# Kernel tuning notes

Hardware: AMD Instinct MI355X
Metric: run time of the kernel (lower is better)

## Reference

```python
import jax, jax.numpy as jnp
import numpy as np

EPS = 1e-5

def conv2d(x, w, b=None, pad=0):
    # x: NCHW, w: OIHW
    y = jax.lax.conv_general_dilated(x, w, (1, 1), [(pad, pad), (pad, pad)],
                                     dimension_numbers=('NCHW', 'OIHW', 'NCHW'))
    if b is not None:
        y = y + b[None, :, None, None]
    return y

def bn(x, g, beta, mean, var):
    scale = g / jnp.sqrt(var + EPS)
    return x * scale[None, :, None, None] + (beta - mean * scale)[None, :, None, None]

def conv_block(x, w, b, g, beta, mean, var):
    # two (conv3x3 + BN + ReLU) stages, params stacked on leading dim 2
    for i in range(2):
        x = jax.nn.relu(bn(conv2d(x, w[i], b[i], pad=1), g[i], beta[i], mean[i], var[i]))
    return x


def setup_inputs() -> dict:
    key = jax.random.key(0)
    ks = jax.random.split(key, 24)
    C, B, H, W = 128, 4, 56, 56
    f32 = jnp.float32
    d = {}
    d['x1'] = jax.random.normal(ks[0], (B, C, H, W), f32)
    d['x2'] = jax.random.normal(ks[1], (B, 4 * C, H, W), f32)
    d['ws'] = jax.random.normal(ks[2], (C, 4 * C, 3, 3), f32) * 0.05
    d['bs'] = jax.random.normal(ks[3], (C,), f32) * 0.05
    d['sg'] = jax.random.uniform(ks[4], (C,), f32)
    d['sbeta'] = jax.random.normal(ks[5], (C,), f32) * 0.05
    d['smean'] = jax.random.normal(ks[6], (C,), f32) * 0.05
    d['svar'] = jax.random.uniform(ks[7], (C,), f32)
    d['wq1'] = jax.random.normal(ks[8], (C, C, 1, 1), f32) * 0.05
    d['wq2'] = jax.random.normal(ks[9], (C, C, 1, 1), f32) * 0.05
    d['v1w'] = jax.random.normal(ks[10], (2, C, C, 3, 3), f32) * 0.05
    d['v1b'] = jax.random.normal(ks[11], (2, C), f32) * 0.05
    d['v1g'] = jax.random.uniform(ks[12], (2, C), f32)
    d['v1beta'] = jax.random.normal(ks[13], (2, C), f32) * 0.05
    d['v1mean'] = jax.random.normal(ks[14], (2, C), f32) * 0.05
    d['v1var'] = jax.random.uniform(ks[15], (2, C), f32)
    d['v2w'] = jax.random.normal(ks[16], (2, C, C, 3, 3), f32) * 0.05
    d['v2b'] = jax.random.normal(ks[17], (2, C), f32) * 0.05
    d['v2g'] = jax.random.uniform(ks[18], (2, C), f32)
    d['v2beta'] = jax.random.normal(ks[19], (2, C), f32) * 0.05
    d['v2mean'] = jax.random.normal(ks[20], (2, C), f32) * 0.05
    d['v2var'] = jax.random.uniform(ks[21], (2, C), f32)
    return d


def reference(x1, x2, ws, bs, sg, sbeta, smean, svar, wq1, wq2,
              v1w, v1b, v1g, v1beta, v1mean, v1var,
              v2w, v2b, v2g, v2beta, v2mean, v2var):
    x2_o = x2
    # conv_s: conv3x3 (4C->C) + BN + ReLU
    x2 = jax.nn.relu(bn(conv2d(x2, ws, bs, pad=1), sg, sbeta, smean, svar))
    B_, C, H, W = x1.shape
    N = H * W
    x1_q = conv2d(x1, wq1)              # [B,C,H,W]
    x2_q = conv2d(x2, wq2)
    x1_v = conv_block(x1, v1w, v1b, v1g, v1beta, v1mean, v1var)
    x2_v = conv_block(x2, v2w, v2b, v2g, v2beta, v2mean, v2var)
    x1_q_flat = x1_q.reshape(B_, C, N)
    x2_q_flat = x2_q.reshape(B_, C, N)
    x2_v_flat = x2_v.reshape(B_, C, N)
    # A[b,n,m] = sum_c x1_q[b,c,n] * x2_q[b,c,m]   -> [B, N1, N2]
    A = jnp.einsum('bcn,bcm->bnm', x1_q_flat, x2_q_flat)
    A = jax.nn.softmax(A, axis=1)                 # softmax over N1 (dim=1)
    # B = softmax(A^T, dim=1) == softmax over N2, then transposed -> [B, N2, N1]
    Bmat = jnp.swapaxes(jax.nn.softmax(A, axis=2), 1, 2)
    # x1_att = bmm(x2_v_flat [B,C,N2], Bmat [B,N2,N1]) -> [B,C,N1]
    x1_att = jnp.einsum('bcm,bmn->bcn', x2_v_flat, Bmat).reshape(B_, C, H, W)
    input1_att = x1_att + x1
    input2_att = x2_o
    return (input1_att, input2_att)
```

## Files before the change

### kernel.cpp

```cpp
#include <hip/hip_runtime.h>
#include <cstdint>
#include <cstddef>

using bfr8 = __attribute__((ext_vector_type(8))) short;
using sh4  = __attribute__((ext_vector_type(4))) short;
using fx4  = __attribute__((ext_vector_type(4))) float;

#define DI __device__ __forceinline__
#define MFMA16(a,b,c) __builtin_amdgcn_mfma_f32_16x16x32_bf16((a),(b),(c),0,0,0)

DI short f2bf(float f){
  unsigned u = __float_as_uint(f);
  return (short)((u + 0x7fffu + ((u >> 16) & 1u)) >> 16);
}
DI float bf2f(short s){
  return __uint_as_float(((unsigned)(unsigned short)s) << 16);
}
DI fx4 fzero(){ fx4 z; z[0]=0.f; z[1]=0.f; z[2]=0.f; z[3]=0.f; return z; }

__global__ void prep_kernel(
    const float* __restrict__ x1, const float* __restrict__ x2,
    const float* __restrict__ wsw, const float* __restrict__ bs,
    const float* __restrict__ sg, const float* __restrict__ sbeta,
    const float* __restrict__ smean, const float* __restrict__ svar,
    const float* __restrict__ wq1, const float* __restrict__ wq2,
    const float* __restrict__ v2w, const float* __restrict__ v2bias,
    const float* __restrict__ v2g, const float* __restrict__ v2beta,
    const float* __restrict__ v2mean, const float* __restrict__ v2var,
    short* __restrict__ x2bf, short* __restrict__ x1T,
    short* __restrict__ wsbf, short* __restrict__ wv2a, short* __restrict__ wv2b,
    short* __restrict__ wq1b, short* __restrict__ wq2b,
    float* __restrict__ consts, float* __restrict__ out1copy)
{
  const int gsz = gridDim.x * blockDim.x;
  const int gid = blockIdx.x * blockDim.x + threadIdx.x;

  for (int i = gid; i < 1605632; i += gsz){
    float4 v = ((const float4*)x2)[i];
    ((float4*)out1copy)[i] = v;
    sh4 o; o[0]=f2bf(v.x); o[1]=f2bf(v.y); o[2]=f2bf(v.z); o[3]=f2bf(v.w);
    ((sh4*)x2bf)[i] = o;
  }
  for (int t = gid; t < 200704; t += gsz){
    int g = t & 15; int nn = t >> 4;
    int b = nn / 3136, n = nn - b*3136;
    bfr8 o;
    #pragma unroll
    for (int k = 0; k < 8; ++k)
      o[k] = f2bf(x1[(size_t)(b*128 + g*8 + k)*3136 + n]);
    *(bfr8*)&x1T[((size_t)(b*3136) + n)*128 + g*8] = o;
  }
  for (int i = gid; i < 589824; i += gsz){
    int ci = i & 511; int tap = (i >> 9) % 9; int co = i / 4608;
    wsbf[i] = f2bf(wsw[(size_t)(co*512 + ci)*9 + tap]);
  }
  for (int i = gid; i < 294912; i += gsz){
    int s = i / 147456; int r = i - s*147456;
    int ci = r & 127; int tap = (r >> 7) % 9; int co = r / 1152;
    float v = v2w[(size_t)((s*128 + co)*128 + ci)*9 + tap];
    (s ? wv2b : wv2a)[r] = f2bf(v);
  }
  for (int i = gid; i < 16384; i += gsz){
    wq1b[i] = f2bf(wq1[i]); wq2b[i] = f2bf(wq2[i]);
  }
  for (int c = gid; c < 128; c += gsz){
    float a = sg[c] * rsqrtf(svar[c] + 1e-5f);
    consts[c]       = a;
    consts[128 + c] = (bs[c] - smean[c]) * a + sbeta[c];
    float a0 = v2g[c] * rsqrtf(v2var[c] + 1e-5f);
    consts[256 + c] = a0;
    consts[384 + c] = (v2bias[c] - v2mean[c]) * a0 + v2beta[c];
    float a1 = v2g[128+c] * rsqrtf(v2var[128+c] + 1e-5f);
    consts[512 + c] = a1;
    consts[640 + c] = (v2bias[128+c] - v2mean[128+c]) * a1 + v2beta[128+c];
  }
}

template<int CIN, int NCIB>
__global__ __launch_bounds__(256, 2) void conv3x3_split_kernel(
    const short* __restrict__ xin, const short* __restrict__ wt,
    float* __restrict__ pout)
{
  __shared__ short xs[4*58*40];
  __shared__ short wsh[9*64*40];

  const int tid = threadIdx.x;
  const int w = tid >> 6, lane = tid & 63, l15 = lane & 15, blk = lane >> 4;
  const int bid = blockIdx.x;
  const int rt = bid % 28, cog = (bid / 28) & 1, b = bid / 56;
  const int r0 = rt * 2;
  const int split = blockIdx.y;
  const int cib0 = split * NCIB;
  float* pbase = pout + (size_t)split * 1605632;

  int pixoff[7];
  #pragma unroll
  for (int pf = 0; pf < 7; ++pf){
    int p = pf*16 + l15;
    int pr = (p >= 56) ? 1 : 0;
    int pc = p - pr*56;
    pixoff[pf] = (pr*58 + pc)*40 + 8*blk;
  }
  const int wlo = (w*16 + l15)*40 + 8*blk;

  fx4 acc[7];
  #pragma unroll
  for (int pf = 0; pf < 7; ++pf) acc[pf] = fzero();

  for (int ci = 0; ci < NCIB; ++ci){
    const int cib = cib0 + ci;
    __syncthreads();
    #pragma unroll
    for (int it = 0; it < 4; ++it){
      int q = it*256 + tid;
      if (q < 928){
        int col = q % 58; int cg8 = (q/58) & 3; int r = q / 232;
        int grow = r0 - 1 + r;
        int gcol = col - 1;
        bfr8 v;
        if (grow >= 0 && grow < 56 && gcol >= 0 && gcol < 56){
          #pragma unroll
          for (int k = 0; k < 8; ++k)
            v[k] = xin[(size_t)(b*CIN + cib*32 + cg8*8 + k)*3136 + grow*56 + gcol];
        } else {
          #pragma unroll
          for (int k = 0; k < 8; ++k) v[k] = 0;
        }
        *(bfr8*)&xs[(r*58 + col)*40 + cg8*8] = v;
      }
    }
    #pragma unroll
    for (int it = 0; it < 9; ++it){
      int q = it*256 + tid;
      int jj = q & 3; int tap = (q >> 2) % 9; int co = q / 36;
      bfr8 wv = *(const bfr8*)&wt[(size_t)((cog*64 + co)*9 + tap)*CIN + cib*32 + jj*8];
      *(bfr8*)&wsh[(tap*64 + co)*40 + jj*8] = wv;
    }
    __syncthreads();
    #pragma unroll
    for (int tap = 0; tap < 9; ++tap){
      bfr8 af = *(const bfr8*)&wsh[tap*64*40 + wlo];
      const int toff = ((tap/3)*58 + (tap%3))*40;
      #pragma unroll
      for (int pf = 0; pf < 7; ++pf){
        bfr8 bf = *(const bfr8*)&xs[pixoff[pf] + toff];
        acc[pf] = MFMA16(af, bf, acc[pf]);
      }
    }
  }
  #pragma unroll
  for (int rr = 0; rr < 4; ++rr){
    int co = cog*64 + w*16 + 4*blk + rr;
    #pragma unroll
    for (int pf = 0; pf < 7; ++pf){
      int n = r0*56 + pf*16 + l15;
      pbase[(size_t)(b*128 + co)*3136 + n] = acc[pf][rr];
    }
  }
}

template<int NS, bool TSTORE>
__global__ __launch_bounds__(256, 4) void conv_combine_kernel(
    const float* __restrict__ p, const float* __restrict__ alpha,
    const float* __restrict__ bconst,
    short* __restrict__ yout, short* __restrict__ youtT)
{
  __shared__ short lt[64][66];
  const int t = threadIdx.x;
  const int bid = blockIdx.x;
  const int nt = bid % 49, cog = (bid / 49) & 1, b = bid / 98;
  const int co0 = cog*64, n0 = nt*64;
  const int coL = t >> 4, ncL = (t & 15) * 4;

  #pragma unroll
  for (int rep = 0; rep < 4; ++rep){
    int co = co0 + rep*16 + coL;
    size_t base = ((size_t)(b*128) + co)*3136 + n0 + ncL;
    float4 s = *(const float4*)&p[base];
    #pragma unroll
    for (int sp = 1; sp < NS; ++sp){
      float4 a = *(const float4*)&p[(size_t)sp*1605632 + base];
      s.x += a.x; s.y += a.y; s.z += a.z; s.w += a.w;
    }
    float al = alpha[co], bc = bconst[co];
    sh4 o;
    o[0] = f2bf(fmaxf(s.x*al + bc, 0.f));
    o[1] = f2bf(fmaxf(s.y*al + bc, 0.f));
    o[2] = f2bf(fmaxf(s.z*al + bc, 0.f));
    o[3] = f2bf(fmaxf(s.w*al + bc, 0.f));
    *(sh4*)&yout[base] = o;
    if (TSTORE) *(sh4*)&lt[rep*16 + coL][ncL] = o;
  }
  if (TSTORE){
    __syncthreads();
    #pragma unroll
    for (int rep = 0; rep < 4; ++rep){
      int nn = rep*16 + (t >> 4);
      int coc = (t & 15) * 4;
      sh4 v;
      #pragma unroll
      for (int j = 0; j < 4; ++j) v[j] = lt[coc + j][nn];
      *(sh4*)&youtT[((size_t)(b*3136) + n0 + nn)*128 + co0 + coc] = v;
    }
  }
}

template<int CIN, bool TSTORE>
__global__ __launch_bounds__(256, 2) void conv3x3_kernel(
    const short* __restrict__ xin, const short* __restrict__ wt,
    const float* __restrict__ alpha, const float* __restrict__ bconst,
    short* __restrict__ yout, short* __restrict__ youtT)
{
  __shared__ short xs[4*58*40];
  __shared__ short wsh[9*64*40];

  const int tid = threadIdx.x;
  const int w = tid >> 6, lane = tid & 63, l15 = lane & 15, blk = lane >> 4;
  const int bid = blockIdx.x;
  const int rt = bid % 28, cog = (bid / 28) & 1, b = bid / 56;
  const int r0 = rt * 2;

  int pixoff[7];
  #pragma unroll
  for (int pf = 0; pf < 7; ++pf){
    int p = pf*16 + l15;
    int pr = (p >= 56) ? 1 : 0;
    int pc = p - pr*56;
    pixoff[pf] = (pr*58 + pc)*40 + 8*blk;
  }
  const int wlo = (w*16 + l15)*40 + 8*blk;

  fx4 acc[7];
  #pragma unroll
  for (int pf = 0; pf < 7; ++pf) acc[pf] = fzero();

  for (int cib = 0; cib < CIN/32; ++cib){
    __syncthreads();
    #pragma unroll
    for (int it = 0; it < 4; ++it){
      int q = it*256 + tid;
      if (q < 928){
        int col = q % 58; int cg8 = (q/58) & 3; int r = q / 232;
        int grow = r0 - 1 + r;
        int gcol = col - 1;
        bfr8 v;
        if (grow >= 0 && grow < 56 && gcol >= 0 && gcol < 56){
          #pragma unroll
          for (int k = 0; k < 8; ++k)
            v[k] = xin[(size_t)(b*CIN + cib*32 + cg8*8 + k)*3136 + grow*56 + gcol];
        } else {
          #pragma unroll
          for (int k = 0; k < 8; ++k) v[k] = 0;
        }
        *(bfr8*)&xs[(r*58 + col)*40 + cg8*8] = v;
      }
    }
    #pragma unroll
    for (int it = 0; it < 9; ++it){
      int q = it*256 + tid;
      int jj = q & 3; int tap = (q >> 2) % 9; int co = q / 36;
      bfr8 wv = *(const bfr8*)&wt[(size_t)((cog*64 + co)*9 + tap)*CIN + cib*32 + jj*8];
      *(bfr8*)&wsh[(tap*64 + co)*40 + jj*8] = wv;
    }
    __syncthreads();
    #pragma unroll
    for (int tap = 0; tap < 9; ++tap){
      bfr8 af = *(const bfr8*)&wsh[tap*64*40 + wlo];
      const int toff = ((tap/3)*58 + (tap%3))*40;
      #pragma unroll
      for (int pf = 0; pf < 7; ++pf){
        bfr8 bf = *(const bfr8*)&xs[pixoff[pf] + toff];
        acc[pf] = MFMA16(af, bf, acc[pf]);
      }
    }
  }
  #pragma unroll
  for (int rr = 0; rr < 4; ++rr){
    int co = cog*64 + w*16 + 4*blk + rr;
    float al = alpha[co], bc = bconst[co];
    #pragma unroll
    for (int pf = 0; pf < 7; ++pf){
      float v = fmaxf(acc[pf][rr]*al + bc, 0.f);
      short sv = f2bf(v);
      int n = r0*56 + pf*16 + l15;
      yout[(size_t)(b*128 + co)*3136 + n] = sv;
// ... 50 lines not shown
      qa[mf][ks] = *(const bfr8*)&q2t[((size_t)(b*3136) + m0 + mf*16 + l15)*128 + ks*32 + 8*blk];

  float vmax[4][4], vsum[4][4];
  #pragma unroll
  for (int mf = 0; mf < 4; ++mf)
    #pragma unroll
    for (int rr = 0; rr < 4; ++rr){ vmax[mf][rr] = -1e30f; vsum[mf][rr] = 0.f; }

  bfr8 qb[4], qbn[4];
  #pragma unroll
  for (int ks = 0; ks < 4; ++ks)
    qb[ks] = *(const bfr8*)&q1t[((size_t)(b*3136) + ns*784 + w*16 + l15)*128 + ks*32 + 8*blk];

  for (int c = w; c < 49; c += 4){
    const int cn = c + 4;
    if (cn < 49){
      #pragma unroll
      for (int ks = 0; ks < 4; ++ks)
        qbn[ks] = *(const bfr8*)&q1t[((size_t)(b*3136) + ns*784 + cn*16 + l15)*128 + ks*32 + 8*blk];
    }
    fx4 acc[4];
    #pragma unroll
    for (int mf = 0; mf < 4; ++mf) acc[mf] = fzero();
    #pragma unroll
    for (int ks = 0; ks < 4; ++ks)
      #pragma unroll
      for (int mf = 0; mf < 4; ++mf)
        acc[mf] = MFMA16(qa[mf][ks], qb[ks], acc[mf]);
    #pragma unroll
    for (int mf = 0; mf < 4; ++mf)
      #pragma unroll
      for (int rr = 0; rr < 4; ++rr){
        float s = acc[mf][rr];
        float nm = fmaxf(vmax[mf][rr], s);
        vsum[mf][rr] = vsum[mf][rr]*__expf(vmax[mf][rr]-nm) + __expf(s-nm);
        vmax[mf][rr] = nm;
      }
    #pragma unroll
    for (int ks = 0; ks < 4; ++ks) qb[ks] = qbn[ks];
  }
  #pragma unroll
  for (int d = 1; d < 16; d <<= 1){
    #pragma unroll
    for (int mf = 0; mf < 4; ++mf)
      #pragma unroll
      for (int rr = 0; rr < 4; ++rr){
        float om = __shfl_xor(vmax[mf][rr], d);
        float os = __shfl_xor(vsum[mf][rr], d);
        float M = fmaxf(vmax[mf][rr], om);
        vsum[mf][rr] = vsum[mf][rr]*__expf(vmax[mf][rr]-M) + os*__expf(om-M);
        vmax[mf][rr] = M;
      }
  }
  if (l15 == 0){
    const size_t base = ((size_t)(b*16 + ns*4 + w))*3136 + m0;
    #pragma unroll
    for (int mf = 0; mf < 4; ++mf)
      #pragma unroll
      for (int rr = 0; rr < 4; ++rr){
        pmax[base + mf*16 + 4*blk + rr] = vmax[mf][rr];
        psum[base + mf*16 + 4*blk + rr] = vsum[mf][rr];
      }
  }
}

__global__ void lse_merge_kernel(
    const float* __restrict__ pmax, const float* __restrict__ psum,
    float* __restrict__ Lm)
{
  int t = blockIdx.x*256 + threadIdx.x;
  if (t >= 12544) return;
  int b = t / 3136, m = t - b*3136;
  float M = -1e30f;
  #pragma unroll
  for (int r = 0; r < 16; ++r)
    M = fmaxf(M, pmax[((size_t)(b*16 + r))*3136 + m]);
  float S = 0.f;
  #pragma unroll
  for (int r = 0; r < 16; ++r){
    size_t i = ((size_t)(b*16 + r))*3136 + m;
    S += psum[i]*__expf(pmax[i] - M);
  }
  Lm[t] = M + __logf(S);
}

__global__ __launch_bounds__(256, 3) void attn3_kernel(
    const short* __restrict__ q1t, const short* __restrict__ q2t,
    const short* __restrict__ x2v, const float* __restrict__ Lm,
    float* __restrict__ part, float* __restrict__ rpart)
{
  __shared__ short q2sh[64*128];
  __shared__ short xsh[128*64];
  __shared__ short plds[4*16*72];
  __shared__ float lmsh[448];
  const int tid = threadIdx.x, w = tid >> 6, lane = tid & 63;
  const int l15 = lane & 15, blk = lane >> 4;
  const int bid = blockIdx.x;
  const int ms = bid % 7, nt = (bid / 7) % 49, b = bid / 343;
  const int m0 = ms*448;
  const int n0w = nt*64 + w*16;

  if (tid < 112)
    ((float4*)lmsh)[tid] = ((const float4*)(Lm + b*3136 + m0))[tid];

  bfr8 qb[4];
  #pragma unroll
  for (int ks = 0; ks < 4; ++ks)
    qb[ks] = *(const bfr8*)&q1t[((size_t)(b*3136) + n0w + l15)*128 + ks*32 + 8*blk];

  bfr8 stq[4], stx[4];
  auto issue = [&](int m0c){
    #pragma unroll
    for (int j = 0; j < 4; ++j){
      int u = tid + 256*j;
      stq[j] = *(const bfr8*)&q2t[((size_t)(b*3136) + m0c + (u>>4))*128 + (u&15)*8];
      stx[j] = *(const bfr8*)&x2v[((size_t)(b*128) + (u>>3))*3136 + m0c + (u&7)*8];
    }
  };
  auto write_stage = [&](){
    #pragma unroll
    for (int j = 0; j < 4; ++j){
      int u = tid + 256*j;
      int qrow = u >> 4;
      *(bfr8*)((char*)q2sh + ((qrow*256 + (u&15)*16) ^ ((qrow&7)<<4))) = stq[j];
      int xrow = u >> 3;
      *(bfr8*)((char*)xsh + ((xrow*128 + (u&7)*16) ^ ((xrow&7)<<4))) = stx[j];
    }
  };

  fx4 pacc[8];
  #pragma unroll
  for (int cf = 0; cf < 8; ++cf) pacc[cf] = fzero();
  float rsum = 0.f;

  issue(m0);

  for (int c = 0; c < 7; ++c){
    __syncthreads();
    write_stage();
    if (c < 6) issue(m0 + (c+1)*64);
    __syncthreads();

    fx4 acc[4];
    #pragma unroll
    for (int mf = 0; mf < 4; ++mf) acc[mf] = fzero();
    #pragma unroll
    for (int ks = 0; ks < 4; ++ks){
      #pragma unroll
      for (int mf = 0; mf < 4; ++mf){
        const int row = mf*16 + l15;
        bfr8 qv = *(const bfr8*)((const char*)q2sh +
                    ((row*256 + ks*64 + 16*blk) ^ ((row&7)<<4)));
        acc[mf] = MFMA16(qv, qb[ks], acc[mf]);
      }
    }

    #pragma unroll
    for (int mf = 0; mf < 4; ++mf){
      fx4 lv = *(const fx4*)&lmsh[c*64 + mf*16 + 4*blk];
      sh4 pk;
      #pragma unroll
      for (int rr = 0; rr < 4; ++rr){
        float a1 = __expf(acc[mf][rr] - lv[rr]);
        float p  = __expf(a1);
        rsum += p;
        pk[rr] = f2bf(p);
      }
      *(sh4*)&plds[(w*16 + l15)*72 + mf*16 + 4*blk] = pk;
    }
    #pragma unroll
    for (int ks2 = 0; ks2 < 2; ++ks2){
      bfr8 pb = *(const bfr8*)&plds[(w*16 + l15)*72 + ks2*32 + 8*blk];
      #pragma unroll
      for (int cf = 0; cf < 8; ++cf){
        const int row = cf*16 + l15;
        bfr8 av = *(const bfr8*)((const char*)xsh +
                    ((row*128 + ks2*64 + 16*blk) ^ ((row&7)<<4)));
        pacc[cf] = MFMA16(av, pb, pacc[cf]);
      }
    }
  }

  rsum += __shfl_xor(rsum, 16);
  rsum += __shfl_xor(rsum, 32);
  if (lane < 16)
    rpart[((size_t)(ms*4 + b))*3136 + n0w + l15] = rsum;

  #pragma unroll
  for (int cf = 0; cf < 8; ++cf)
    #pragma unroll
    for (int rr = 0; rr < 4; ++rr){
      int cc = cf*16 + 4*blk + rr;
      part[(((size_t)(ms*4 + b))*128 + cc)*3136 + n0w + l15] = pacc[cf][rr];
    }
}

__global__ void rtot_kernel(const float* __restrict__ rpart,
                            float* __restrict__ rinv)
{
  int t = blockIdx.x*256 + threadIdx.x;
  if (t >= 12544) return;
  int b = t / 3136, n = t - b*3136;
  float s = 0.f;
  #pragma unroll
  for (int ms = 0; ms < 7; ++ms)
    s += rpart[((size_t)(ms*4 + b))*3136 + n];
  rinv[t] = 1.0f / s;
}

__global__ __launch_bounds__(256, 8) void attn_combine_kernel(
    const float* __restrict__ part, const float* __restrict__ rinv,
    const float* __restrict__ x1, float* __restrict__ out0)
{
  int t = blockIdx.x*256 + threadIdx.x;
  int n4 = t % 784; int rest = t / 784;
  int cc = rest & 127; int b = rest >> 7;
  const float4* p4 = (const float4*)part;
  float4 s = {0.f,0.f,0.f,0.f};
  #pragma unroll
  for (int ms = 0; ms < 7; ++ms){
    float4 v = p4[(((size_t)(ms*4 + b))*128 + cc)*784 + n4];
    s.x += v.x; s.y += v.y; s.z += v.z; s.w += v.w;
  }
  float4 rv = ((const float4*)rinv)[b*784 + n4];
  size_t xi = ((size_t)(b*128) + cc)*784 + n4;
  float4 xv = ((const float4*)x1)[xi];
  float4 o;
  o.x = s.x*rv.x + xv.x; o.y = s.y*rv.y + xv.y;
  o.z = s.z*rv.z + xv.z; o.w = s.w*rv.w + xv.w;
  ((float4*)out0)[xi] = o;
}

__global__ __launch_bounds__(256, 2) void colstats_kernel(
    const short* __restrict__ q1t, const short* __restrict__ q2t,
    float* __restrict__ Lm)
{
  __shared__ float smax[4][16];
  __shared__ float ssum[4][16];
  const int tid = threadIdx.x, w = tid >> 6, lane = tid & 63;
  const int l15 = lane & 15, blk = lane >> 4;
  const int b = blockIdx.x / 196, m0 = (blockIdx.x % 196) * 16;

  bfr8 bfr[4];
  #pragma unroll
  for (int ks = 0; ks < 4; ++ks)
    bfr[ks] = *(const bfr8*)&q2t[((size_t)(b*3136) + m0 + l15)*128 + ks*32 + 8*blk];

  float vmax = -1e30f, vsum = 0.f;

  for (int nc = w; nc < 196; nc += 4){
    fx4 acc = fzero();
    #pragma unroll
    for (int ks = 0; ks < 4; ++ks){
      bfr8 af = *(const bfr8*)&q1t[((size_t)(b*3136) + nc*16 + l15)*128 + ks*32 + 8*blk];
      acc = MFMA16(af, bfr[ks], acc);
// ... 108 lines not shown
      int c = cf*16 + 4*blk + rr;
      size_t idx = (size_t)(b*128 + c)*3136 + n;
      out0[idx] = v*rinv + x1[idx];
    }
  }
}

extern "C" void kernel_launch(void* const* d_in, const int* in_sizes, int n_in,
                              void* d_out, int out_size, void* d_ws, size_t ws_size,
                              hipStream_t stream)
{
  (void)in_sizes; (void)n_in; (void)out_size;
  const float* x1     = (const float*)d_in[0];
  const float* x2     = (const float*)d_in[1];
  const float* wsw    = (const float*)d_in[2];
  const float* bs     = (const float*)d_in[3];
  const float* sg     = (const float*)d_in[4];
  const float* sbeta  = (const float*)d_in[5];
  const float* smean  = (const float*)d_in[6];
  const float* svar   = (const float*)d_in[7];
  const float* wq1    = (const float*)d_in[8];
  const float* wq2    = (const float*)d_in[9];
  const float* v2w    = (const float*)d_in[16];
  const float* v2bias = (const float*)d_in[17];
  const float* v2g    = (const float*)d_in[18];
  const float* v2beta = (const float*)d_in[19];
  const float* v2mean = (const float*)d_in[20];
  const float* v2var  = (const float*)d_in[21];

  char* ws = (char*)d_ws;
  auto al = [](size_t x){ return (x + 255) & ~(size_t)255; };

  const size_t sz_nc    = al((size_t)1605632*2);
  const size_t sz_x2bf  = al((size_t)6422528*2);
  const size_t sz_Lm    = al((size_t)12544*4);
  const size_t sz_lsep  = al((size_t)16*12544*4);
  const size_t sz_rp    = al((size_t)28*12544*4);
  const size_t sz_cst   = al((size_t)768*4);
  const size_t sz_part  = al((size_t)7*1605632*4);
  const size_t sz_wsbf  = al((size_t)589824*2);
  const size_t sz_wv2   = al((size_t)147456*2);
  const size_t sz_wq    = al((size_t)16384*2);

  short *x2bf, *x1T, *wsbf, *wv2a, *wv2b, *wq1b, *wq2b;
  short *x2s, *x2sT, *q1t, *q2t, *v2t, *x2v;
  float *consts, *Lm;
  float *pmax = nullptr, *psum = nullptr, *part = nullptr;
  float *rpart = nullptr, *rinv = nullptr, *pbuf = nullptr;

  size_t off = 0;
  const size_t o_x2v = off;  off += sz_nc;
  const size_t o_q1t = off;  off += sz_nc;
  const size_t o_q2t = off;  off += sz_nc;
  const size_t o_Lm  = off;  off += sz_Lm;
  const size_t o_pmx = off;  off += sz_lsep;
  const size_t o_psm = off;  off += sz_lsep;
  const size_t o_rp  = off;  off += sz_rp;
  const size_t o_ri  = off;  off += sz_Lm;
  const size_t o_cst = off;  off += sz_cst;
  const size_t o_prt = off;  off += sz_part;
  const size_t o_x2b = off;  off += sz_x2bf;
  const size_t o_x1T = off;  off += sz_nc;
  const size_t o_xsT = off;  off += sz_nc;
  const size_t o_x2s = off;  off += sz_nc;
  const size_t o_v2t = off;  off += sz_nc;
  const size_t o_wsb = off;  off += sz_wsbf;
  const size_t o_wva = off;  off += sz_wv2;
  const size_t o_wvb = off;  off += sz_wv2;
  const size_t o_wq1 = off;  off += sz_wq;
  const size_t o_wq2 = off;  off += sz_wq;
  const size_t fast_need = off;
  const bool fast = (ws_size >= fast_need);

  if (fast){
    x2v    = (short*)(ws + o_x2v);
    q1t    = (short*)(ws + o_q1t);
    q2t    = (short*)(ws + o_q2t);
    Lm     = (float*)(ws + o_Lm);
    pmax   = (float*)(ws + o_pmx);
    psum   = (float*)(ws + o_psm);
    rpart  = (float*)(ws + o_rp);
    rinv   = (float*)(ws + o_ri);
    consts = (float*)(ws + o_cst);
    part   = (float*)(ws + o_prt);
    pbuf   = (float*)(ws + o_prt);
    x2bf   = (short*)(ws + o_x2b);
    x1T    = (short*)(ws + o_x1T);
    x2sT   = (short*)(ws + o_xsT);
    x2s    = (short*)(ws + o_x2s);
    v2t    = (short*)(ws + o_v2t);
    wsbf   = (short*)(ws + o_wsb);
    wv2a   = (short*)(ws + o_wva);
    wv2b   = (short*)(ws + o_wvb);
    wq1b   = (short*)(ws + o_wq1);
    wq2b   = (short*)(ws + o_wq2);
  } else {
    size_t o = 0;
    auto bump = [&](size_t bytes)->char*{ char* p = ws + o; o += al(bytes); return p; };
    x2bf   = (short*)bump((size_t)6422528*2);
    x1T    = (short*)bump((size_t)1605632*2);
    wsbf   = (short*)bump((size_t)589824*2);
    wv2a   = (short*)bump((size_t)147456*2);
    wv2b   = (short*)bump((size_t)147456*2);
    wq1b   = (short*)bump((size_t)16384*2);
    wq2b   = (short*)bump((size_t)16384*2);
    consts = (float*)bump((size_t)768*4);
    x2s    = (short*)bump((size_t)1605632*2);
    x2sT   = (short*)bump((size_t)1605632*2);
    q1t    = (short*)bump((size_t)1605632*2);
    q2t    = (short*)bump((size_t)1605632*2);
    v2t    = (short*)bump((size_t)1605632*2);
    x2v    = (short*)bump((size_t)1605632*2);
    Lm     = (float*)bump((size_t)12544*4);
  }

  float* out0 = (float*)d_out;
  float* out1 = out0 + 1605632;

  prep_kernel<<<2048, 256, 0, stream>>>(x1, x2, wsw, bs, sg, sbeta, smean, svar,
      wq1, wq2, v2w, v2bias, v2g, v2beta, v2mean, v2var,
      x2bf, x1T, wsbf, wv2a, wv2b, wq1b, wq2b, consts, out1);

  if (fast){
    conv3x3_split_kernel<512, 4><<<dim3(224,4), 256, 0, stream>>>(x2bf, wsbf, pbuf);
    conv_combine_kernel<4, true ><<<392, 256, 0, stream>>>(pbuf, consts,       consts + 128, x2s, x2sT);
    qproj_kernel<<<784, 256, 0, stream>>>(x1T,  wq1b, q1t);
    qproj_kernel<<<784, 256, 0, stream>>>(x2sT, wq2b, q2t);
    conv3x3_split_kernel<128, 2><<<dim3(224,2), 256, 0, stream>>>(x2s, wv2a, pbuf);
    conv_combine_kernel<2, false><<<392, 256, 0, stream>>>(pbuf, consts + 256, consts + 384, v2t, nullptr);
    conv3x3_split_kernel<128, 2><<<dim3(224,2), 256, 0, stream>>>(v2t, wv2b, pbuf);
    conv_combine_kernel<2, false><<<392, 256, 0, stream>>>(pbuf, consts + 512, consts + 640, x2v, nullptr);
    lse_kernel<<<784, 256, 0, stream>>>(q1t, q2t, pmax, psum);
    lse_merge_kernel<<<49, 256, 0, stream>>>(pmax, psum, Lm);
    attn3_kernel<<<1372, 256, 0, stream>>>(q1t, q2t, x2v, Lm, part, rpart);
    rtot_kernel<<<49, 256, 0, stream>>>(rpart, rinv);
    attn_combine_kernel<<<1568, 256, 0, stream>>>(part, rinv, x1, out0);
  } else {
    conv3x3_kernel<512, true ><<<224, 256, 0, stream>>>(x2bf, wsbf, consts, consts + 128, x2s, x2sT);
    qproj_kernel<<<784, 256, 0, stream>>>(x1T,  wq1b, q1t);
    qproj_kernel<<<784, 256, 0, stream>>>(x2sT, wq2b, q2t);
    conv3x3_kernel<128, false><<<224, 256, 0, stream>>>(x2s, wv2a, consts + 256, consts + 384, v2t, nullptr);
    conv3x3_kernel<128, false><<<224, 256, 0, stream>>>(v2t, wv2b, consts + 512, consts + 640, x2v, nullptr);
    colstats_kernel<<<784, 256, 0, stream>>>(q1t, q2t, Lm);
    attn_kernel<<<784, 256, 0, stream>>>(q1t, q2t, x2v, Lm, x1, out0);
  }
}
```

Baseline: 216.1 us.

## Use channel-last bf16 activations for convs and bf16 attention partials

```diff
diff --git a/kernel.cpp b/kernel.cpp
--- a/kernel.cpp
+++ b/kernel.cpp
@@ -17,6 +17,8 @@
   return __uint_as_float(((unsigned)(unsigned short)s) << 16);
 }
 DI fx4 fzero(){ fx4 z; z[0]=0.f; z[1]=0.f; z[2]=0.f; z[3]=0.f; return z; }
+DI bfr8 bzero(){ bfr8 z; 
+  z[0]=0; z[1]=0; z[2]=0; z[3]=0; z[4]=0; z[5]=0; z[6]=0; z[7]=0; return z; }
 
 __global__ void prep_kernel(
     const float* __restrict__ x1, const float* __restrict__ x2,
@@ -30,7 +32,7 @@
     short* __restrict__ x2bf, short* __restrict__ x1T,
     short* __restrict__ wsbf, short* __restrict__ wv2a, short* __restrict__ wv2b,
     short* __restrict__ wq1b, short* __restrict__ wq2b,
-    float* __restrict__ consts, float* __restrict__ out1copy)
+    float* __restrict__ consts, float* __restrict__ out1copy, int legacy)
 {
   const int gsz = gridDim.x * blockDim.x;
   const int gid = blockIdx.x * blockDim.x + threadIdx.x;
@@ -38,17 +40,21 @@
   for (int i = gid; i < 1605632; i += gsz){
     float4 v = ((const float4*)x2)[i];
     ((float4*)out1copy)[i] = v;
-    sh4 o; o[0]=f2bf(v.x); o[1]=f2bf(v.y); o[2]=f2bf(v.z); o[3]=f2bf(v.w);
-    ((sh4*)x2bf)[i] = o;
-  }
-  for (int t = gid; t < 200704; t += gsz){
-    int g = t & 15; int nn = t >> 4;
-    int b = nn / 3136, n = nn - b*3136;
-    bfr8 o;
-    #pragma unroll
-    for (int k = 0; k < 8; ++k)
-      o[k] = f2bf(x1[(size_t)(b*128 + g*8 + k)*3136 + n]);
-    *(bfr8*)&x1T[((size_t)(b*3136) + n)*128 + g*8] = o;
+    if (legacy){
+      sh4 o; o[0]=f2bf(v.x); o[1]=f2bf(v.y); o[2]=f2bf(v.z); o[3]=f2bf(v.w);
+      ((sh4*)x2bf)[i] = o;
+    }
+  }
+  if (legacy){
+    for (int t = gid; t < 200704; t += gsz){
+      int g = t & 15; int nn = t >> 4;
+      int b = nn / 3136, n = nn - b*3136;
+      bfr8 o;
+      #pragma unroll
+      for (int k = 0; k < 8; ++k)
+        o[k] = f2bf(x1[(size_t)(b*128 + g*8 + k)*3136 + n]);
+      *(bfr8*)&x1T[((size_t)(b*3136) + n)*128 + g*8] = o;
+    }
   }
   for (int i = gid; i < 589824; i += gsz){
     int ci = i & 511; int tap = (i >> 9) % 9; int co = i / 4608;
@@ -76,9 +82,37 @@
   }
 }
 
+template<int C>
+__global__ __launch_bounds__(256, 4) void transpose_cn_kernel(
+    const float* __restrict__ in, short* __restrict__ out)
+{
+  __shared__ float t[32][65];
+  const int tid = threadIdx.x, bid = blockIdx.x;
+  const int nt = bid % 49, cg = (bid / 49) % (C/32), b = bid / (49*(C/32));
+  const int n0 = nt*64, c0 = cg*32;
+
+  #pragma unroll
+  for (int j = 0; j < 2; ++j){
+    int u = tid + 256*j;
+    int row = u >> 4, col4 = u & 15;
+    float4 v = *(const float4*)&in[((size_t)(b*C) + c0 + row)*3136 + n0 + col4*4];
+    t[row][col4*4+0] = v.x; t[row][col4*4+1] = v.y;
+    t[row][col4*4+2] = v.z; t[row][col4*4+3] = v.w;
+  }
+  __syncthreads();
+  {
+    int n = tid >> 2, cg8 = tid & 3;
+    bfr8 o;
+    #pragma unroll
+    for (int k = 0; k < 8; ++k) o[k] = f2bf(t[cg8*8 + k][n]);
+    *(bfr8*)&out[((size_t)(b*3136) + n0 + n)*C + c0 + cg8*8] = o;
+  }
+}
+
 template<int CIN, int NCIB>
 __global__ __launch_bounds__(256, 2) void conv3x3_split_kernel(
-    const short* __restrict__ xin, const short* __restrict__ wt,
+    const short* __restrict__ xin,
+    const short* __restrict__ wt,
     float* __restrict__ pout)
 {
   __shared__ short xs[4*58*40];
@@ -89,9 +123,8 @@
   const int bid = blockIdx.x;
   const int rt = bid % 28, cog = (bid / 28) & 1, b = bid / 56;
   const int r0 = rt * 2;
-  const int split = blockIdx.y;
-  const int cib0 = split * NCIB;
-  float* pbase = pout + (size_t)split * 1605632;
+  const int cib0 = blockIdx.y * NCIB;
+  float* pbase = pout + (size_t)blockIdx.y * 1605632;
 
   int pixoff[7];
   #pragma unroll
@@ -103,12 +136,145 @@
   }
   const int wlo = (w*16 + l15)*40 + 8*blk;
 
+  int in_act[4], in_val[4], in_lds[4], in_go[4];
+  #pragma unroll
+  for (int it = 0; it < 4; ++it){
+    int q = it*256 + tid;
+    int cg8 = q & 3, col = (q >> 2) % 58, r = q / 232;
+    int grow = r0 - 1 + r, gcol = col - 1;
+    in_act[it] = (q < 928);
+    in_val[it] = in_act[it] && grow >= 0 && grow < 56 && gcol >= 0 && gcol < 56;
+    in_lds[it] = (r*58 + col)*40 + cg8*8;
+    int gr = in_val[it] ? grow : 0, gc = in_val[it] ? gcol : 0;
+    in_go[it] = (b*3136 + gr*56 + gc)*CIN + cib0*32 + cg8*8;
+  }
+  int wt_lds[9], wt_go[9];
+  #pragma unroll
+  for (int it = 0; it < 9; ++it){
+    int q = it*256 + tid;
+    int jj = q & 3, tap = (q >> 2) % 9, co = q / 36;
+    wt_lds[it] = (tap*64 + co)*40 + jj*8;
+    wt_go[it] = ((cog*64 + co)*9 + tap)*CIN + cib0*32 + jj*8;
+  }
+
   fx4 acc[7];
   #pragma unroll
   for (int pf = 0; pf < 7; ++pf) acc[pf] = fzero();
 
   for (int ci = 0; ci < NCIB; ++ci){
-    const int cib = cib0 + ci;
+    __syncthreads();
+    #pragma unroll
+    for (int it = 0; it < 4; ++it){
+      if (in_act[it]){
+        bfr8 v = bzero();
+        if (in_val[it]) v = *(const bfr8*)&xin[in_go[it]];
+        *(bfr8*)&xs[in_lds[it]] = v;
+        in_go[it] += 32;
+      }
+    }
+    #pragma unroll
+    for (int it = 0; it < 9; ++it){
+      *(bfr8*)&wsh[wt_lds[it]] = *(const bfr8*)&wt[wt_go[it]];
+      wt_go[it] += 32;
+    }
+    __syncthreads();
+    #pragma unroll
+    for (int tap = 0; tap < 9; ++tap){
+      bfr8 af = *(const bfr8*)&wsh[tap*64*40 + wlo];
+      const int toff = ((tap/3)*58 + (tap%3))*40;
+      #pragma unroll
+      for (int pf = 0; pf < 7; ++pf){
+        bfr8 bf = *(const bfr8*)&xs[pixoff[pf] + toff];
+        acc[pf] = MFMA16(af, bf, acc[pf]);
+      }
+    }
+  }
+  #pragma unroll
+  for (int rr = 0; rr < 4; ++rr){
+    int co = cog*64 + w*16 + 4*blk + rr;
+    #pragma unroll
+    for (int pf = 0; pf < 7; ++pf){
+      int n = r0*56 + pf*16 + l15;
+      pbase[(size_t)(b*128 + co)*3136 + n] = acc[pf][rr];
+    }
+  }
+}
+
+template<int NS, int MODE>
+__global__ __launch_bounds__(256, 4) void conv_combine_kernel(
+    const float* __restrict__ p, const float* __restrict__ alpha,
+    const float* __restrict__ bconst, short* __restrict__ yout)
+{
+  __shared__ short lt[64][66];
+  const int t = threadIdx.x;
+  const int bid = blockIdx.x;
+  const int nt = bid % 49, cog = (bid / 49) & 1, b = bid / 98;
+  const int co0 = cog*64, n0 = nt*64;
+  const int coL = t >> 4, ncL = (t & 15) * 4;
+
+  #pragma unroll
+  for (int rep = 0; rep < 4; ++rep){
+    int co = co0 + rep*16 + coL;
+    size_t base = ((size_t)(b*128) + co)*3136 + n0 + ncL;
+    float4 s = *(const float4*)&p[base];
+    #pragma unroll
+    for (int sp = 1; sp < NS; ++sp){
+      float4 a = *(const float4*)&p[(size_t)sp*1605632 + base];
+      s.x += a.x; s.y += a.y; s.z += a.z; s.w += a.w;
+    }
+    float al = alpha[co], bc = bconst[co];
+    sh4 o;
+    o[0] = f2bf(fmaxf(s.x*al + bc, 0.f));
+    o[1] = f2bf(fmaxf(s.y*al + bc, 0.f));
+    o[2] = f2bf(fmaxf(s.z*al + bc, 0.f));
+    o[3] = f2bf(fmaxf(s.w*al + bc, 0.f));
+    if (MODE == 0) *(sh4*)&yout[base] = o;
+    else           *(sh4*)&lt[rep*16 + coL][ncL] = o;
+  }
+  if (MODE == 1){
+    __syncthreads();
+    #pragma unroll
+    for (int rep = 0; rep < 4; ++rep){
+      int nn = rep*16 + (t >> 4);
+      int coc = (t & 15) * 4;
+      sh4 v;
+      #pragma unroll
+      for (int j = 0; j < 4; ++j) v[j] = lt[coc + j][nn];
+      *(sh4*)&yout[((size_t)(b*3136) + n0 + nn)*128 + co0 + coc] = v;
+    }
+  }
+}
+
+template<int CIN, bool TSTORE>
+__global__ __launch_bounds__(256, 2) void conv3x3_kernel(
+    const short* __restrict__ xin, const short* __restrict__ wt,
+    const float* __restrict__ alpha, const float* __restrict__ bconst,
+    short* __restrict__ yout, short* __restrict__ youtT)
+{
+  __shared__ short xs[4*58*40];
+  __shared__ short wsh[9*64*40];
+
+  const int tid = threadIdx.x;
+  const int w = tid >> 6, lane = tid & 63, l15 = lane & 15, blk = lane >> 4;
+  const int bid = blockIdx.x;
+  const int rt = bid % 28, cog = (bid / 28) & 1, b = bid / 56;
+  const int r0 = rt * 2;
+
+  int pixoff[7];
+  #pragma unroll
+  for (int pf = 0; pf < 7; ++pf){
+    int p = pf*16 + l15;
+    int pr = (p >= 56) ? 1 : 0;
+    int pc = p - pr*56;
+    pixoff[pf] = (pr*58 + pc)*40 + 8*blk;
+  }
+  const int wlo = (w*16 + l15)*40 + 8*blk;
+
+  fx4 acc[7];
+  #pragma unroll
+  for (int pf = 0; pf < 7; ++pf) acc[pf] = fzero();
+
+  for (int cib = 0; cib < CIN/32; ++cib){
     __syncthreads();
     #pragma unroll
     for (int it = 0; it < 4; ++it){
@@ -117,140 +283,11 @@
         int col = q % 58; int cg8 = (q/58) & 3; int r = q / 232;
         int grow = r0 - 1 + r;
         int gcol = col - 1;
-        bfr8 v;
+        bfr8 v = bzero();
         if (grow >= 0 && grow < 56 && gcol >= 0 && gcol < 56){
           #pragma unroll
           for (int k = 0; k < 8; ++k)
             v[k] = xin[(size_t)(b*CIN + cib*32 + cg8*8 + k)*3136 + grow*56 + gcol];
-        } else {
-          #pragma unroll
-          for (int k = 0; k < 8; ++k) v[k] = 0;
-        }
-        *(bfr8*)&xs[(r*58 + col)*40 + cg8*8] = v;
-      }
-    }
-    #pragma unroll
-    for (int it = 0; it < 9; ++it){
-      int q = it*256 + tid;
-      int jj = q & 3; int tap = (q >> 2) % 9; int co = q / 36;
-      bfr8 wv = *(const bfr8*)&wt[(size_t)((cog*64 + co)*9 + tap)*CIN + cib*32 + jj*8];
-      *(bfr8*)&wsh[(tap*64 + co)*40 + jj*8] = wv;
-    }
-    __syncthreads();
-    #pragma unroll
-    for (int tap = 0; tap < 9; ++tap){
-      bfr8 af = *(const bfr8*)&wsh[tap*64*40 + wlo];
-      const int toff = ((tap/3)*58 + (tap%3))*40;
-      #pragma unroll
-      for (int pf = 0; pf < 7; ++pf){
-        bfr8 bf = *(const bfr8*)&xs[pixoff[pf] + toff];
-        acc[pf] = MFMA16(af, bf, acc[pf]);
-      }
-    }
-  }
-  #pragma unroll
-  for (int rr = 0; rr < 4; ++rr){
-    int co = cog*64 + w*16 + 4*blk + rr;
-    #pragma unroll
-    for (int pf = 0; pf < 7; ++pf){
-      int n = r0*56 + pf*16 + l15;
-      pbase[(size_t)(b*128 + co)*3136 + n] = acc[pf][rr];
-    }
-  }
-}
-
-template<int NS, bool TSTORE>
-__global__ __launch_bounds__(256, 4) void conv_combine_kernel(
-    const float* __restrict__ p, const float* __restrict__ alpha,
-    const float* __restrict__ bconst,
-    short* __restrict__ yout, short* __restrict__ youtT)
-{
-  __shared__ short lt[64][66];
-  const int t = threadIdx.x;
-  const int bid = blockIdx.x;
-  const int nt = bid % 49, cog = (bid / 49) & 1, b = bid / 98;
-  const int co0 = cog*64, n0 = nt*64;
-  const int coL = t >> 4, ncL = (t & 15) * 4;
-
-  #pragma unroll
-  for (int rep = 0; rep < 4; ++rep){
-    int co = co0 + rep*16 + coL;
-    size_t base = ((size_t)(b*128) + co)*3136 + n0 + ncL;
-    float4 s = *(const float4*)&p[base];
-    #pragma unroll
-    for (int sp = 1; sp < NS; ++sp){
-      float4 a = *(const float4*)&p[(size_t)sp*1605632 + base];
-      s.x += a.x; s.y += a.y; s.z += a.z; s.w += a.w;
-    }
-    float al = alpha[co], bc = bconst[co];
-    sh4 o;
-    o[0] = f2bf(fmaxf(s.x*al + bc, 0.f));
-    o[1] = f2bf(fmaxf(s.y*al + bc, 0.f));
-    o[2] = f2bf(fmaxf(s.z*al + bc, 0.f));
-    o[3] = f2bf(fmaxf(s.w*al + bc, 0.f));
-    *(sh4*)&yout[base] = o;
-    if (TSTORE) *(sh4*)&lt[rep*16 + coL][ncL] = o;
-  }
-  if (TSTORE){
-    __syncthreads();
-    #pragma unroll
-    for (int rep = 0; rep < 4; ++rep){
-      int nn = rep*16 + (t >> 4);
-      int coc = (t & 15) * 4;
-      sh4 v;
-      #pragma unroll
-      for (int j = 0; j < 4; ++j) v[j] = lt[coc + j][nn];
-      *(sh4*)&youtT[((size_t)(b*3136) + n0 + nn)*128 + co0 + coc] = v;
-    }
-  }
-}
-
-template<int CIN, bool TSTORE>
-__global__ __launch_bounds__(256, 2) void conv3x3_kernel(
-    const short* __restrict__ xin, const short* __restrict__ wt,
-    const float* __restrict__ alpha, const float* __restrict__ bconst,
-    short* __restrict__ yout, short* __restrict__ youtT)
-{
-  __shared__ short xs[4*58*40];
-  __shared__ short wsh[9*64*40];
-
-  const int tid = threadIdx.x;
-  const int w = tid >> 6, lane = tid & 63, l15 = lane & 15, blk = lane >> 4;
-  const int bid = blockIdx.x;
-  const int rt = bid % 28, cog = (bid / 28) & 1, b = bid / 56;
-  const int r0 = rt * 2;
-
-  int pixoff[7];
-  #pragma unroll
-  for (int pf = 0; pf < 7; ++pf){
-    int p = pf*16 + l15;
-    int pr = (p >= 56) ? 1 : 0;
-    int pc = p - pr*56;
-    pixoff[pf] = (pr*58 + pc)*40 + 8*blk;
-  }
-  const int wlo = (w*16 + l15)*40 + 8*blk;
-
-  fx4 acc[7];
-  #pragma unroll
-  for (int pf = 0; pf < 7; ++pf) acc[pf] = fzero();
-
-  for (int cib = 0; cib < CIN/32; ++cib){
-    __syncthreads();
-    #pragma unroll
-    for (int it = 0; it < 4; ++it){
-      int q = it*256 + tid;
-      if (q < 928){
-        int col = q % 58; int cg8 = (q/58) & 3; int r = q / 232;
-        int grow = r0 - 1 + r;
-        int gcol = col - 1;
-        bfr8 v;
-        if (grow >= 0 && grow < 56 && gcol >= 0 && gcol < 56){
-          #pragma unroll
-          for (int k = 0; k < 8; ++k)
-            v[k] = xin[(size_t)(b*CIN + cib*32 + cg8*8 + k)*3136 + grow*56 + gcol];
-        } else {
-          #pragma unroll
-          for (int k = 0; k < 8; ++k) v[k] = 0;
         }
         *(bfr8*)&xs[(r*58 + col)*40 + cg8*8] = v;
       }
@@ -367,9 +404,13 @@
       #pragma unroll
       for (int rr = 0; rr < 4; ++rr){
         float s = acc[mf][rr];
-        float nm = fmaxf(vmax[mf][rr], s);
-        vsum[mf][rr] = vsum[mf][rr]*__expf(vmax[mf][rr]-nm) + __expf(s-nm);
-        vmax[mf][rr] = nm;
+        float d = s - vmax[mf][rr];
+        float e = __expf(-fabsf(d));
+        bool up = d > 0.f;
+        float mlt = up ? e : 1.f;
+        float add = up ? 1.f : e;
+        vsum[mf][rr] = vsum[mf][rr]*mlt + add;
+        vmax[mf][rr] = fmaxf(vmax[mf][rr], s);
       }
     #pragma unroll
     for (int ks = 0; ks < 4; ++ks) qb[ks] = qbn[ks];
@@ -419,14 +460,14 @@
   Lm[t] = M + __logf(S);
 }
 
-__global__ __launch_bounds__(256, 3) void attn3_kernel(
+__global__ __launch_bounds__(256, 4) void attn3_kernel(
     const short* __restrict__ q1t, const short* __restrict__ q2t,
     const short* __restrict__ x2v, const float* __restrict__ Lm,
-    float* __restrict__ part, float* __restrict__ rpart)
-{
-  __shared__ short q2sh[64*128];
-  __shared__ short xsh[128*64];
-  __shared__ short plds[4*16*72];
+    short* __restrict__ part, float* __restrict__ rpart)
+{
+  __shared__ short q2sh[32*128];
+  __shared__ short xsh[128*32];
+  __shared__ short plds[4*16*40];
   __shared__ float lmsh[448];
   const int tid = threadIdx.x, w = tid >> 6, lane = tid & 63;
   const int l15 = lane & 15, blk = lane >> 4;
@@ -443,23 +484,23 @@
   for (int ks = 0; ks < 4; ++ks)
     qb[ks] = *(const bfr8*)&q1t[((size_t)(b*3136) + n0w + l15)*128 + ks*32 + 8*blk];
 
-  bfr8 stq[4], stx[4];
+  bfr8 stq[2], stx[2];
   auto issue = [&](int m0c){
     #pragma unroll
-    for (int j = 0; j < 4; ++j){
+    for (int j = 0; j < 2; ++j){
       int u = tid + 256*j;
       stq[j] = *(const bfr8*)&q2t[((size_t)(b*3136) + m0c + (u>>4))*128 + (u&15)*8];
-      stx[j] = *(const bfr8*)&x2v[((size_t)(b*128) + (u>>3))*3136 + m0c + (u&7)*8];
+      stx[j] = *(const bfr8*)&x2v[((size_t)(b*128) + (u>>2))*3136 + m0c + (u&3)*8];
     }
   };
   auto write_stage = [&](){
     #pragma unroll
-    for (int j = 0; j < 4; ++j){
+    for (int j = 0; j < 2; ++j){
       int u = tid + 256*j;
       int qrow = u >> 4;
       *(bfr8*)((char*)q2sh + ((qrow*256 + (u&15)*16) ^ ((qrow&7)<<4))) = stq[j];
-      int xrow = u >> 3;
-      *(bfr8*)((char*)xsh + ((xrow*128 + (u&7)*16) ^ ((xrow&7)<<4))) = stx[j];
+      int xrow = u >> 2;
+      *(bfr8*)((char*)xsh + ((xrow*64 + (u&3)*16) ^ ((xrow&7)<<4))) = stx[j];
     }
   };
 
@@ -470,19 +511,18 @@
 
   issue(m0);
 
-  for (int c = 0; c < 7; ++c){
+  for (int c = 0; c < 14; ++c){
     __syncthreads();
     write_stage();
-    if (c < 6) issue(m0 + (c+1)*64);
+    if (c < 13) issue(m0 + (c+1)*32);
     __syncthreads();
 
-    fx4 acc[4];
-    #pragma unroll
-    for (int mf = 0; mf < 4; ++mf) acc[mf] = fzero();
+    fx4 acc[2];
+    acc[0] = fzero(); acc[1] = fzero();
     #pragma unroll
     for (int ks = 0; ks < 4; ++ks){
       #pragma unroll
-      for (int mf = 0; mf < 4; ++mf){
+      for (int mf = 0; mf < 2; ++mf){
         const int row = mf*16 + l15;
         bfr8 qv = *(const bfr8*)((const char*)q2sh +
                     ((row*256 + ks*64 + 16*blk) ^ ((row&7)<<4)));
@@ -491,8 +531,8 @@
     }
 
     #pragma unroll
-    for (int mf = 0; mf < 4; ++mf){
-      fx4 lv = *(const fx4*)&lmsh[c*64 + mf*16 + 4*blk];
+    for (int mf = 0; mf < 2; ++mf){
+      fx4 lv = *(const fx4*)&lmsh[c*32 + mf*16 + 4*blk];
       sh4 pk;
       #pragma unroll
       for (int rr = 0; rr < 4; ++rr){
@@ -501,18 +541,15 @@
         rsum += p;
         pk[rr] = f2bf(p);
       }
-      *(sh4*)&plds[(w*16 + l15)*72 + mf*16 + 4*blk] = pk;
-    }
-    #pragma unroll
-    for (int ks2 = 0; ks2 < 2; ++ks2){
-      bfr8 pb = *(const bfr8*)&plds[(w*16 + l15)*72 + ks2*32 + 8*blk];
-      #pragma unroll
-      for (int cf = 0; cf < 8; ++cf){
-        const int row = cf*16 + l15;
-        bfr8 av = *(const bfr8*)((const char*)xsh +
-                    ((row*128 + ks2*64 + 16*blk) ^ ((row&7)<<4)));
-        pacc[cf] = MFMA16(av, pb, pacc[cf]);
-      }
+      *(sh4*)&plds[(w*16 + l15)*40 + mf*16 + 4*blk] = pk;
+    }
+    bfr8 pb = *(const bfr8*)&plds[(w*16 + l15)*40 + 8*blk];
+    #pragma unroll
+    for (int cf = 0; cf < 8; ++cf){
+      const int row = cf*16 + l15;
+      bfr8 av = *(const bfr8*)((const char*)xsh +
+                  ((row*64 + 16*blk) ^ ((row&7)<<4)));
+      pacc[cf] = MFMA16(av, pb, pacc[cf]);
     }
   }
 
@@ -526,7 +563,7 @@
     #pragma unroll
     for (int rr = 0; rr < 4; ++rr){
       int cc = cf*16 + 4*blk + rr;
-      part[(((size_t)(ms*4 + b))*128 + cc)*3136 + n0w + l15] = pacc[cf][rr];
+      part[(((size_t)(ms*4 + b))*128 + cc)*3136 + n0w + l15] = f2bf(pacc[cf][rr]);
     }
 }
 
@@ -544,18 +581,17 @@
 }
 
 __global__ __launch_bounds__(256, 8) void attn_combine_kernel(
-    const float* __restrict__ part, const float* __restrict__ rinv,
+    const short* __restrict__ part, const float* __restrict__ rinv,
     const float* __restrict__ x1, float* __restrict__ out0)
 {
   int t = blockIdx.x*256 + threadIdx.x;
   int n4 = t % 784; int rest = t / 784;
   int cc = rest & 127; int b = rest >> 7;
-  const float4* p4 = (const float4*)part;
   float4 s = {0.f,0.f,0.f,0.f};
   #pragma unroll
   for (int ms = 0; ms < 7; ++ms){
-    float4 v = p4[(((size_t)(ms*4 + b))*128 + cc)*784 + n4];
-    s.x += v.x; s.y += v.y; s.z += v.z; s.w += v.w;
+    sh4 v = *(const sh4*)&part[((((size_t)(ms*4 + b))*128 + cc)*3136) + n4*4];
+    s.x += bf2f(v[0]); s.y += bf2f(v[1]); s.z += bf2f(v[2]); s.w += bf2f(v[3]);
   }
   float4 rv = ((const float4*)rinv)[b*784 + n4];
   size_t xi = ((size_t)(b*128) + cc)*784 + n4;
@@ -730,110 +766,107 @@
   auto al = [](size_t x){ return (x + 255) & ~(size_t)255; };
 
   const size_t sz_nc    = al((size_t)1605632*2);
-  const size_t sz_x2bf  = al((size_t)6422528*2);
+  const size_t sz_x2T   = al((size_t)6422528*2);
   const size_t sz_Lm    = al((size_t)12544*4);
   const size_t sz_lsep  = al((size_t)16*12544*4);
   const size_t sz_rp    = al((size_t)28*12544*4);
   const size_t sz_cst   = al((size_t)768*4);
-  const size_t sz_part  = al((size_t)7*1605632*4);
+  const size_t sz_part  = al((size_t)7*1605632*2);
+  const size_t sz_pbuf  = al((size_t)4*1605632*4);
   const size_t sz_wsbf  = al((size_t)589824*2);
   const size_t sz_wv2   = al((size_t)147456*2);
   const size_t sz_wq    = al((size_t)16384*2);
-
-  short *x2bf, *x1T, *wsbf, *wv2a, *wv2b, *wq1b, *wq2b;
-  short *x2s, *x2sT, *q1t, *q2t, *v2t, *x2v;
-  float *consts, *Lm;
-  float *pmax = nullptr, *psum = nullptr, *part = nullptr;
-  float *rpart = nullptr, *rinv = nullptr, *pbuf = nullptr;
 
   size_t off = 0;
   const size_t o_x2v = off;  off += sz_nc;
   const size_t o_q1t = off;  off += sz_nc;
   const size_t o_q2t = off;  off += sz_nc;
+  const size_t o_x1T = off;  off += sz_nc;
+  const size_t o_x2s = off;  off += sz_nc;
+  const size_t o_v2t = off;  off += sz_nc;
   const size_t o_Lm  = off;  off += sz_Lm;
   const size_t o_pmx = off;  off += sz_lsep;
   const size_t o_psm = off;  off += sz_lsep;
   const size_t o_rp  = off;  off += sz_rp;
   const size_t o_ri  = off;  off += sz_Lm;
   const size_t o_cst = off;  off += sz_cst;
-  const size_t o_prt = off;  off += sz_part;
-  const size_t o_x2b = off;  off += sz_x2bf;
-  const size_t o_x1T = off;  off += sz_nc;
-  const size_t o_xsT = off;  off += sz_nc;
-  const size_t o_x2s = off;  off += sz_nc;
-  const size_t o_v2t = off;  off += sz_nc;
   const size_t o_wsb = off;  off += sz_wsbf;
   const size_t o_wva = off;  off += sz_wv2;
   const size_t o_wvb = off;  off += sz_wv2;
   const size_t o_wq1 = off;  off += sz_wq;
   const size_t o_wq2 = off;  off += sz_wq;
+  const size_t o_x2T = off;  off += sz_x2T;
+  const size_t o_prt = off;  off += (sz_part > sz_pbuf ? sz_part : sz_pbuf);
   const size_t fast_need = off;
   const bool fast = (ws_size >= fast_need);
 
-  if (fast){
-    x2v    = (short*)(ws + o_x2v);
-    q1t    = (short*)(ws + o_q1t);
-    q2t    = (short*)(ws + o_q2t);
-    Lm     = (float*)(ws + o_Lm);
-    pmax   = (float*)(ws + o_pmx);
-    psum   = (float*)(ws + o_psm);
-    rpart  = (float*)(ws + o_rp);
-    rinv   = (float*)(ws + o_ri);
-    consts = (float*)(ws + o_cst);
-    part   = (float*)(ws + o_prt);
-    pbuf   = (float*)(ws + o_prt);
-    x2bf   = (short*)(ws + o_x2b);
-    x1T    = (short*)(ws + o_x1T);
-    x2sT   = (short*)(ws + o_xsT);
-    x2s    = (short*)(ws + o_x2s);
-    v2t    = (short*)(ws + o_v2t);
-    wsbf   = (short*)(ws + o_wsb);
-    wv2a   = (short*)(ws + o_wva);
-    wv2b   = (short*)(ws + o_wvb);
-    wq1b   = (short*)(ws + o_wq1);
-    wq2b   = (short*)(ws + o_wq2);
-  } else {
-    size_t o = 0;
-    auto bump = [&](size_t bytes)->char*{ char* p = ws + o; o += al(bytes); return p; };
-    x2bf   = (short*)bump((size_t)6422528*2);
-    x1T    = (short*)bump((size_t)1605632*2);
-    wsbf   = (short*)bump((size_t)589824*2);
-    wv2a   = (short*)bump((size_t)147456*2);
-    wv2b   = (short*)bump((size_t)147456*2);
-    wq1b   = (short*)bump((size_t)16384*2);
-    wq2b   = (short*)bump((size_t)16384*2);
-    consts = (float*)bump((size_t)768*4);
-    x2s    = (short*)bump((size_t)1605632*2);
-    x2sT   = (short*)bump((size_t)1605632*2);
-    q1t    = (short*)bump((size_t)1605632*2);
-    q2t    = (short*)bump((size_t)1605632*2);
-    v2t    = (short*)bump((size_t)1605632*2);
-    x2v    = (short*)bump((size_t)1605632*2);
-    Lm     = (float*)bump((size_t)12544*4);
-  }
-
   float* out0 = (float*)d_out;
   float* out1 = out0 + 1605632;
 
-  prep_kernel<<<2048, 256, 0, stream>>>(x1, x2, wsw, bs, sg, sbeta, smean, svar,
-      wq1, wq2, v2w, v2bias, v2g, v2beta, v2mean, v2var,
-      x2bf, x1T, wsbf, wv2a, wv2b, wq1b, wq2b, consts, out1);
-
   if (fast){
-    conv3x3_split_kernel<512, 4><<<dim3(224,4), 256, 0, stream>>>(x2bf, wsbf, pbuf);
-    conv_combine_kernel<4, true ><<<392, 256, 0, stream>>>(pbuf, consts,       consts + 128, x2s, x2sT);
-    qproj_kernel<<<784, 256, 0, stream>>>(x1T,  wq1b, q1t);
-    qproj_kernel<<<784, 256, 0, stream>>>(x2sT, wq2b, q2t);
+    short* x2v  = (short*)(ws + o_x2v);
+    short* q1t  = (short*)(ws + o_q1t);
+    short* q2t  = (short*)(ws + o_q2t);
+    short* x1T  = (short*)(ws + o_x1T);
+    short* x2s  = (short*)(ws + o_x2s);
+    short* v2t  = (short*)(ws + o_v2t);
+    float* Lm   = (float*)(ws + o_Lm);
+    float* pmax = (float*)(ws + o_pmx);
+    float* psum = (float*)(ws + o_psm);
+    float* rpart= (float*)(ws + o_rp);
+    float* rinv = (float*)(ws + o_ri);
+    float* consts = (float*)(ws + o_cst);
+    short* wsbf = (short*)(ws + o_wsb);
+    short* wv2a = (short*)(ws + o_wva);
+    short* wv2b = (short*)(ws + o_wvb);
+    short* wq1b = (short*)(ws + o_wq1);
+    short* wq2b = (short*)(ws + o_wq2);
+    short* x2T  = (short*)(ws + o_x2T);
+    short* part = (short*)(ws + o_prt);
+    float* pbuf = (float*)(ws + o_prt);
+
+    prep_kernel<<<2048, 256, 0, stream>>>(x1, x2, wsw, bs, sg, sbeta, smean, svar,
+        wq1, wq2, v2w, v2bias, v2g, v2beta, v2mean, v2var,
+        nullptr, nullptr, wsbf, wv2a, wv2b, wq1b, wq2b, consts, out1, 0);
+    transpose_cn_kernel<512><<<3136, 256, 0, stream>>>(x2, x2T);
+    transpose_cn_kernel<128><<<784, 256, 0, stream>>>(x1, x1T);
+
+    conv3x3_split_kernel<512, 4><<<dim3(224,4), 256, 0, stream>>>(x2T, wsbf, pbuf);
+    conv_combine_kernel<4, 1><<<392, 256, 0, stream>>>(pbuf, consts,       consts + 128, x2s);
+    qproj_kernel<<<784, 256, 0, stream>>>(x1T, wq1b, q1t);
+    qproj_kernel<<<784, 256, 0, stream>>>(x2s, wq2b, q2t);
     conv3x3_split_kernel<128, 2><<<dim3(224,2), 256, 0, stream>>>(x2s, wv2a, pbuf);
-    conv_combine_kernel<2, false><<<392, 256, 0, stream>>>(pbuf, consts + 256, consts + 384, v2t, nullptr);
+    conv_combine_kernel<2, 1><<<392, 256, 0, stream>>>(pbuf, consts + 256, consts + 384, v2t);
     conv3x3_split_kernel<128, 2><<<dim3(224,2), 256, 0, stream>>>(v2t, wv2b, pbuf);
-    conv_combine_kernel<2, false><<<392, 256, 0, stream>>>(pbuf, consts + 512, consts + 640, x2v, nullptr);
+    conv_combine_kernel<2, 0><<<392, 256, 0, stream>>>(pbuf, consts + 512, consts + 640, x2v);
+
     lse_kernel<<<784, 256, 0, stream>>>(q1t, q2t, pmax, psum);
     lse_merge_kernel<<<49, 256, 0, stream>>>(pmax, psum, Lm);
     attn3_kernel<<<1372, 256, 0, stream>>>(q1t, q2t, x2v, Lm, part, rpart);
     rtot_kernel<<<49, 256, 0, stream>>>(rpart, rinv);
     attn_combine_kernel<<<1568, 256, 0, stream>>>(part, rinv, x1, out0);
   } else {
+    size_t o = 0;
+    auto bump = [&](size_t bytes)->char*{ char* p = ws + o; o += al(bytes); return p; };
+    short* x2bf   = (short*)bump((size_t)6422528*2);
+    short* x1T    = (short*)bump((size_t)1605632*2);
+    short* wsbf   = (short*)bump((size_t)589824*2);
+    short* wv2a   = (short*)bump((size_t)147456*2);
+    short* wv2b   = (short*)bump((size_t)147456*2);
+    short* wq1b   = (short*)bump((size_t)16384*2);
+    short* wq2b   = (short*)bump((size_t)16384*2);
+    float* consts = (float*)bump((size_t)768*4);
+    short* x2s    = (short*)bump((size_t)1605632*2);
+    short* x2sT   = (short*)bump((size_t)1605632*2);
+    short* q1t    = (short*)bump((size_t)1605632*2);
+    short* q2t    = (short*)bump((size_t)1605632*2);
+    short* v2t    = (short*)bump((size_t)1605632*2);
+    short* x2v    = (short*)bump((size_t)1605632*2);
+    float* Lm     = (float*)bump((size_t)12544*4);
+
+    prep_kernel<<<2048, 256, 0, stream>>>(x1, x2, wsw, bs, sg, sbeta, smean, svar,
+        wq1, wq2, v2w, v2bias, v2g, v2beta, v2mean, v2var,
+        x2bf, x1T, wsbf, wv2a, wv2b, wq1b, wq2b, consts, out1, 1);
     conv3x3_kernel<512, true ><<<224, 256, 0, stream>>>(x2bf, wsbf, consts, consts + 128, x2s, x2sT);
     qproj_kernel<<<784, 256, 0, stream>>>(x1T,  wq1b, q1t);
     qproj_kernel<<<784, 256, 0, stream>>>(x2sT, wq2b, q2t);
```

After: 210.3 us. 1.03x faster.
